# Kernel tuning notes

Measured on AMD Instinct MI355X. Metric: run time of the kernel, lower is better.

The kernel has to match this reference:

```python
import jax, jax.numpy as jnp
import numpy as np

N_NODES = 100000
N_EDGES = 1600000
IN_F = 64
HIDDEN = 128
HIDDEN2 = HIDDEN // 2
N_CLASSES = 10


def setup_inputs() -> dict:
    key = jax.random.key(0)
    ks = jax.random.split(key, 8)
    x = jax.random.normal(ks[0], (N_NODES, IN_F), dtype=jnp.float32)
    edge_index = jax.random.randint(ks[1], (2, N_EDGES), 0, N_NODES, dtype=jnp.int64 if jax.config.jax_enable_x64 else jnp.int32)
    # Linear params (PyTorch nn.Linear: y = x @ W.T + b); store as [in, out] for einsum-free matmul
    def lin(k, fi, fo):
        bound = 1.0 / np.sqrt(fi)
        kw, kb = jax.random.split(k)
        W = jax.random.uniform(kw, (fi, fo), minval=-bound, maxval=bound, dtype=jnp.float32)
        b = jax.random.uniform(kb, (fo,), minval=-bound, maxval=bound, dtype=jnp.float32)
        return W, b
    W1, b1 = lin(ks[2], IN_F, HIDDEN)
    W2, b2 = lin(ks[3], HIDDEN, HIDDEN2)
    W3, b3 = lin(ks[4], HIDDEN2, N_CLASSES)
    return {"x": x, "edge_index": edge_index, "n_nodes": N_NODES,
            "W1": W1, "b1": b1, "W2": W2, "b2": b2, "W3": W3, "b3": b3}


def gcn_layer(x, row, col, n_nodes, W, b):
    # gather source features, scatter-add into destination nodes
    agg = jax.ops.segment_sum(x[row], col, num_segments=n_nodes)  # [N, F]
    deg = jax.ops.segment_sum(jnp.ones_like(col, dtype=x.dtype), col, num_segments=n_nodes)
    deg = jnp.maximum(deg, 1.0)
    return (agg / deg[:, None]) @ W + b


def reference(x, edge_index, n_nodes, W1, b1, W2, b2, W3, b3):
    row, col = edge_index[0], edge_index[1]
    h = jax.nn.relu(gcn_layer(x, row, col, n_nodes, W1, b1))
    # dropout is identity in eval mode
    h = jax.nn.relu(gcn_layer(h, row, col, n_nodes, W2, b2))
    return h @ W3 + b3
```

## Files before the change

### kernel.cpp

```cpp
#include <hip/hip_runtime.h>

#define N_NODES 100000
#define N_EDGES 1600000
#define IN_F 64
#define HID 128
#define HID2 64
#define NCLS 10

#define SEG 64

#define NBUCK 256
#define SUBR 391
#define CAP2 7000
#define EBA 1600

typedef __attribute__((ext_vector_type(8))) short bfrag;
typedef __attribute__((ext_vector_type(4))) float f32x4;

__device__ __forceinline__ unsigned short bf_rne(float f) {
  unsigned int u = __float_as_uint(f);
  u += 0x7fffu + ((u >> 16) & 1u);
  return (unsigned short)(u >> 16);
}

__global__ __launch_bounds__(256) void cast_k(const float* __restrict__ x,
                                              unsigned short* __restrict__ xb) {
  int i = blockIdx.x * blockDim.x + threadIdx.x;
  const float4* xf4 = (const float4*)x;
  float4 a = xf4[2 * i];
  float4 b = xf4[2 * i + 1];
  ushort4 o0, o1;
  o0.x = bf_rne(a.x); o0.y = bf_rne(a.y); o0.z = bf_rne(a.z); o0.w = bf_rne(a.w);
  o1.x = bf_rne(b.x); o1.y = bf_rne(b.y); o1.z = bf_rne(b.z); o1.w = bf_rne(b.w);
  ushort4* ob = (ushort4*)xb;
  ob[2 * i] = o0;
  ob[2 * i + 1] = o1;
}

__global__ __launch_bounds__(256) void wtrans_k(const float* __restrict__ W1,
                                                const float* __restrict__ W2,
                                                unsigned short* __restrict__ W1t,
                                                unsigned short* __restrict__ W2t) {
  int i = blockIdx.x * 256 + threadIdx.x;
  if (i < IN_F * HID) {
    int j = i >> 6, k = i & 63;
    W1t[i] = bf_rne(W1[k * HID + j]);
  } else {
    int i2 = i - IN_F * HID;
    int j = i2 >> 7, k = i2 & 127;
    W2t[i2] = bf_rne(W2[k * HID2 + j]);
  }
}

__global__ __launch_bounds__(256) void binA_k(const int* __restrict__ row,
                                              const int* __restrict__ col,
                                              int* __restrict__ bcnt,
                                              unsigned int* __restrict__ pairs) {
  __shared__ int hcnt[NBUCK];
  __shared__ int hbase[NBUCK];
  int t = threadIdx.x;
  hcnt[t] = 0;
  __syncthreads();
  int e0 = blockIdx.x * EBA;
  int e1 = e0 + EBA;
  for (int e = e0 + t; e < e1; e += 256) {
    int b = col[e] / SUBR;
    atomicAdd(&hcnt[b], 1);
  }
  __syncthreads();
  hbase[t] = atomicAdd(&bcnt[t], hcnt[t]);
  hcnt[t] = 0;
  __syncthreads();
  for (int e = e0 + t; e < e1; e += 256) {
    int dst = col[e];
    int src = row[e];
    int b = dst / SUBR;
    int pos = hbase[b] + atomicAdd(&hcnt[b], 1);
    pairs[(size_t)b * CAP2 + pos] =
        ((unsigned)(dst - b * SUBR) << 17) | (unsigned)src;
  }
}

__global__ __launch_bounds__(512) void binB_k(const unsigned int* __restrict__ pairs,
                                              const int* __restrict__ bcnt,
                                              int* __restrict__ cursors,
                                              int* __restrict__ csr_src) {
  __shared__ int cur[SUBR];
  int b = blockIdx.x;
  int t = threadIdx.x;
  int lo = b * SUBR;
  for (int i = t; i < SUBR; i += 512) cur[i] = 0;
  __syncthreads();
  int cnt = bcnt[b];
  const unsigned int* bp = pairs + (size_t)b * CAP2;
  for (int i = t; i < cnt; i += 512) {
    unsigned w = bp[i];
    int local = w >> 17;
    int src = (int)(w & 0x1ffffu);
    int pos = atomicAdd(&cur[local], 1);
    if (pos < SEG) csr_src[(size_t)(lo + local) * SEG + pos] = src;
  }
  __syncthreads();
  for (int i = t; i < SUBR; i += 512) {
    int n = lo + i;
    if (n < N_NODES) {
      int d = cur[i];
      if (d > SEG) d = SEG;
      cursors[n] = n * SEG + d;
      int cons = d <= 32 ? 32 : ((d + 15) & ~15);
      for (int q = d; q < cons; q++) csr_src[(size_t)n * SEG + q] = 0;
    }
  }
}

#define ACC1(r)                                                     \
  {                                                                 \
    ax += __uint_as_float((r).x << 16);                             \
    ay += __uint_as_float((r).x & 0xffff0000u);                     \
    az += __uint_as_float((r).y << 16);                             \
    aw += __uint_as_float((r).y & 0xffff0000u);                     \
  }
#define LD8(r, ia, ib)                                              \
  {                                                                 \
    r[0] = vb[(size_t)(unsigned)(ia).x * 16 + fc];                  \
    r[1] = vb[(size_t)(unsigned)(ia).y * 16 + fc];                  \
    r[2] = vb[(size_t)(unsigned)(ia).z * 16 + fc];                  \
    r[3] = vb[(size_t)(unsigned)(ia).w * 16 + fc];                  \
    r[4] = vb[(size_t)(unsigned)(ib).x * 16 + fc];                  \
    r[5] = vb[(size_t)(unsigned)(ib).y * 16 + fc];                  \
    r[6] = vb[(size_t)(unsigned)(ib).z * 16 + fc];                  \
    r[7] = vb[(size_t)(unsigned)(ib).w * 16 + fc];                  \
  }
#define NODE_BODY(i, rbuf, dd)                                      \
  {                                                                 \
    float ax = 0.f, ay = 0.f, az = 0.f, aw = 0.f;                   \
    ACC1(rbuf[0]) ACC1(rbuf[1]) ACC1(rbuf[2]) ACC1(rbuf[3])         \
    ACC1(rbuf[4]) ACC1(rbuf[5]) ACC1(rbuf[6]) ACC1(rbuf[7])         \
    int cons = 32;                                                  \
    if (dd > 32) {                                                  \
      cons = (dd + 15) & ~15;                                       \
      int sbase = (n0 + i) * SEG;                                   \
      for (int p = sbase + 32; p < sbase + cons; p += 16) {         \
        int4 iT = csr4[(p >> 2) + eg];                              \
        uint2 t0 = vb[(size_t)(unsigned)iT.x * 16 + fc];            \
        uint2 t1 = vb[(size_t)(unsigned)iT.y * 16 + fc];            \
        uint2 t2 = vb[(size_t)(unsigned)iT.z * 16 + fc];            \
        uint2 t3 = vb[(size_t)(unsigned)iT.w * 16 + fc];            \
        ACC1(t0) ACC1(t1) ACC1(t2) ACC1(t3)                         \
      }                                                             \
    }                                                               \
    ax += __shfl_xor(ax, 16); ay += __shfl_xor(ay, 16);             \
    az += __shfl_xor(az, 16); aw += __shfl_xor(aw, 16);             \
    ax += __shfl_xor(ax, 32); ay += __shfl_xor(ay, 32);             \
    az += __shfl_xor(az, 32); aw += __shfl_xor(aw, 32);             \
    float pc = (float)(cons - dd);                                  \
    emit(i, make_float4(ax - pc * zx, ay - pc * zy,                 \
                        az - pc * zz, aw - pc * zw), dd);           \
  }

template <class F>
__device__ __forceinline__ void gather4_bf16(
    const uint2* __restrict__ vb, const int* __restrict__ csr,
    const int* __restrict__ cursors, int n0, int eg, int fc, F&& emit) {
  const int4* csr4 = (const int4*)csr;
  size_t rb = (size_t)n0 * 16;
  int4 iA0 = csr4[rb + eg];
  int4 iB0 = csr4[rb + 4 + eg];
  int4 iA1 = csr4[rb + 16 + eg];
  int4 iB1 = csr4[rb + 20 + eg];
  int4 iA2 = csr4[rb + 32 + eg];
  int4 iB2 = csr4[rb + 36 + eg];
  int4 iA3 = csr4[rb + 48 + eg];
  int4 iB3 = csr4[rb + 52 + eg];
  int d0 = cursors[n0 + 0] - (n0 + 0) * SEG;
  int d1 = cursors[n0 + 1] - (n0 + 1) * SEG;
  int d2 = cursors[n0 + 2] - (n0 + 2) * SEG;
  int d3 = cursors[n0 + 3] - (n0 + 3) * SEG;
  uint2 z = vb[fc];
  uint2 rA[8], rB[8], rC[8], rD[8];
  LD8(rA, iA0, iB0)
  LD8(rB, iA1, iB1)
  LD8(rC, iA2, iB2)
  LD8(rD, iA3, iB3)
  __builtin_amdgcn_sched_barrier(0);
  float zx = __uint_as_float(z.x << 16);
  float zy = __uint_as_float(z.x & 0xffff0000u);
  float zz = __uint_as_float(z.y << 16);
  float zw = __uint_as_float(z.y & 0xffff0000u);
  NODE_BODY(0, rA, d0)
  NODE_BODY(1, rB, d1)
  NODE_BODY(2, rC, d2)
  NODE_BODY(3, rD, d3)
}

#define NB1 32
#define XS_S 72
#define HS_S 136
__global__ __launch_bounds__(512, 4) void gmm1_k(
    const unsigned short* __restrict__ xb, const int* __restrict__ cursors,
    const int* __restrict__ csr_src, const unsigned short* __restrict__ W1t,
    const float* __restrict__ b1, const unsigned short* __restrict__ W2t,
    unsigned short* __restrict__ g) {
  __shared__ unsigned short xsb[NB1 * XS_S];
  __shared__ unsigned short hsb[NB1 * HS_S];
  int t = threadIdx.x;
  int node0 = blockIdx.x * NB1;
  int wave = t >> 6;
  int lane = t & 63;
  int eg = lane >> 4;
  int fc = lane & 15;
  {
    const uint2* vb = (const uint2*)xb;
    gather4_bf16(vb, csr_src, cursors, node0 + wave * 4, eg, fc,
                 [&](int i, float4 a, int dd) {
                   if (eg == 0) {
                     float inv = 1.0f / (dd < 1 ? 1.0f : (float)dd);
                     ushort4 o;
                     o.x = bf_rne(a.x * inv); o.y = bf_rne(a.y * inv);
                     o.z = bf_rne(a.z * inv); o.w = bf_rne(a.w * inv);
                     *(ushort4*)&xsb[(wave * 4 + i) * XS_S + fc * 4] = o;
                   }
                 });
  }
  __syncthreads();
  int lr = lane & 15;
  int kb = lane >> 4;
  {
    int col = wave * 16 + lr;
    bfrag wf0 = *(const bfrag*)&W1t[col * IN_F + kb * 8];
    bfrag wf1 = *(const bfrag*)&W1t[col * IN_F + 32 + kb * 8];
    float bb = b1[col];
#pragma unroll
    for (int m = 0; m < 2; m++) {
      f32x4 acc = {0.f, 0.f, 0.f, 0.f};
      bfrag a0 = *(const bfrag*)&xsb[(m * 16 + lr) * XS_S + kb * 8];
      bfrag a1 = *(const bfrag*)&xsb[(m * 16 + lr) * XS_S + 32 + kb * 8];
      acc = __builtin_amdgcn_mfma_f32_16x16x32_bf16(a0, wf0, acc, 0, 0, 0);
      acc = __builtin_amdgcn_mfma_f32_16x16x32_bf16(a1, wf1, acc, 0, 0, 0);
#pragma unroll
      for (int q = 0; q < 4; q++) {
        int r = m * 16 + kb * 4 + q;
        float v = acc[q] + bb;
        hsb[r * HS_S + col] = bf_rne(v > 0.0f ? v : 0.0f);
      }
    }
  }
  __syncthreads();
  {
    int m = wave >> 2;
    int col = (wave & 3) * 16 + lr;
    f32x4 acc = {0.f, 0.f, 0.f, 0.f};
#pragma unroll
    for (int s = 0; s < 4; s++) {
      bfrag af = *(const bfrag*)&hsb[(m * 16 + lr) * HS_S + s * 32 + kb * 8];
      bfrag bf = *(const bfrag*)&W2t[col * HID + s * 32 + kb * 8];
      acc = __builtin_amdgcn_mfma_f32_16x16x32_bf16(af, bf, acc, 0, 0, 0);
    }
#pragma unroll
    for (int q = 0; q < 4; q++) {
      int r = m * 16 + kb * 4 + q;
      g[(size_t)(node0 + r) * HID2 + col] = bf_rne(acc[q]);
    }
  }
}

#define NBH 32
__global__ __launch_bounds__(512, 4) void ghead_k(
    const unsigned short* __restrict__ g, const int* __restrict__ cursors,
    const int* __restrict__ csr_src, const float* __restrict__ b2,
    const float* __restrict__ W3, const float* __restrict__ b3,
    float* __restrict__ out) {
  __shared__ float W3l[HID2 * NCLS];
  __shared__ float hs[NBH][HID2 + 4];
  int t = threadIdx.x;
  for (int i = t; i < HID2 * NCLS; i += 512) W3l[i] = W3[i];
  int node0 = blockIdx.x * NBH;
  int lane = t & 63;
  int wave = t >> 6;
  int eg = lane >> 4;
  int fc = lane & 15;
  {
    const uint2* vb = (const uint2*)g;
    const float4* b2f4 = (const float4*)b2;
    float4 bb = b2f4[fc];
    gather4_bf16(vb, csr_src, cursors, node0 + wave * 4, eg, fc,
                 [&](int i, float4 a, int dd) {
                   if (eg == 0) {
                     float inv = 1.0f / (dd < 1 ? 1.0f : (float)dd);
                     float4 v;
                     v.x = a.x * inv + bb.x; v.y = a.y * inv + bb.y;
                     v.z = a.z * inv + bb.z; v.w = a.w * inv + bb.w;
                     v.x = v.x > 0.0f ? v.x : 0.0f;
                     v.y = v.y > 0.0f ? v.y : 0.0f;
                     v.z = v.z > 0.0f ? v.z : 0.0f;
                     v.w = v.w > 0.0f ? v.w : 0.0f;
                     *(float4*)&hs[wave * 4 + i][fc * 4] = v;
                   }
                 });
  }
  __syncthreads();
  if (t < NBH * NCLS) {
    int n = t / NCLS;
    int c = t - n * NCLS;
    float a = b3[c];
    for (int k = 0; k < HID2; k++) a += hs[n][k] * W3l[k * NCLS + c];
    out[(size_t)(node0 + n) * NCLS + c] = a;
  }
}

extern "C" void kernel_launch(void* const* d_in, const int* in_sizes, int n_in,
                              void* d_out, int out_size, void* d_ws, size_t ws_size,
                              hipStream_t stream) {
  const float* x  = (const float*)d_in[0];
  const int*   ei = (const int*)d_in[1];
  const int*   row = ei;
  const int*   col = ei + N_EDGES;
  const float* W1 = (const float*)d_in[3];
  const float* b1 = (const float*)d_in[4];
  const float* W2 = (const float*)d_in[5];
  const float* b2 = (const float*)d_in[6];
  const float* W3 = (const float*)d_in[7];
  const float* b3 = (const float*)d_in[8];
  float* out = (float*)d_out;

  char* ws = (char*)d_ws;
  int*            cursors = (int*)ws;
  int*            bcnt    = (int*)(ws + (512 << 10));
  unsigned short* W1t     = (unsigned short*)(ws + (520 << 10));
  unsigned short* W2t     = (unsigned short*)(ws + (552 << 10));
  int*            csr_src = (int*)(ws + (1 << 20));
  unsigned int*   pairs   = (unsigned int*)(ws + (28 << 20));
  unsigned short* xb      = (unsigned short*)(ws + (36 << 20));
  unsigned short* g       = (unsigned short*)(ws + (49 << 20));

  (void)hipMemsetAsync(bcnt, 0, NBUCK * sizeof(int), stream);
  wtrans_k<<<(IN_F * HID + HID * HID2) / 256, 256, 0, stream>>>(W1, W2, W1t, W2t);
  cast_k<<<N_NODES * IN_F / 8 / 256, 256, 0, stream>>>(x, xb);
  binA_k<<<N_EDGES / EBA, 256, 0, stream>>>(row, col, bcnt, pairs);
  binB_k<<<NBUCK, 512, 0, stream>>>(pairs, bcnt, cursors, csr_src);

  gmm1_k<<<N_NODES / NB1, 512, 0, stream>>>(xb, cursors, csr_src, W1t, b1, W2t, g);

  ghead_k<<<N_NODES / NBH, 512, 0, stream>>>(g, cursors, csr_src, b2, W3, b3, out);
}
```

Measured before the change: 157.2 us.

## Split fused gather+matmul kernels into separate gather and dense kernels

Splits the two fused gather+MFMA kernels into standalone gather kernels (256 threads, one node at a time per wave) that write mean-aggregated bf16 features to a workspace buffer, followed by separate matmul and head kernels that read them back. The aim is smaller, higher-occupancy gather kernels without the matmul's shared-memory and register footprint. It also drops the explicit batching of 32 outstanding loads per lane. In exchange it adds two kernel launches and an extra round trip of intermediate features through global memory.

Measured after the change: 166.9 us. 1.06x slower.

```diff
diff --git a/kernel.cpp b/kernel.cpp
--- a/kernel.cpp
+++ b/kernel.cpp
@@ -113,6 +113,23 @@
   }
 }
 
+__device__ __forceinline__ float4 gather_node(const uint2* __restrict__ vb,
+                                              const int4* __restrict__ csr4,
+                                              int n, int d, int eg, int fc,
+                                              float zx, float zy, float zz,
+                                              float zw) {
+  float ax = 0.f, ay = 0.f, az = 0.f, aw = 0.f;
+  int s4 = n * 16;
+  int4 ia = csr4[s4 + eg];
+  int4 ib = csr4[s4 + 4 + eg];
+  uint2 r0 = vb[(size_t)(unsigned)ia.x * 16 + fc];
+  uint2 r1 = vb[(size_t)(unsigned)ia.y * 16 + fc];
+  uint2 r2 = vb[(size_t)(unsigned)ia.z * 16 + fc];
+  uint2 r3 = vb[(size_t)(unsigned)ia.w * 16 + fc];
+  uint2 r4 = vb[(size_t)(unsigned)ib.x * 16 + fc];
+  uint2 r5 = vb[(size_t)(unsigned)ib.y * 16 + fc];
+  uint2 r6 = vb[(size_t)(unsigned)ib.z * 16 + fc];
+  uint2 r7 = vb[(size_t)(unsigned)ib.w * 16 + fc];
 #define ACC1(r)                                                     \
   {                                                                 \
     ax += __uint_as_float((r).x << 16);                             \
@@ -120,109 +137,114 @@
     az += __uint_as_float((r).y << 16);                             \
     aw += __uint_as_float((r).y & 0xffff0000u);                     \
   }
-#define LD8(r, ia, ib)                                              \
-  {                                                                 \
-    r[0] = vb[(size_t)(unsigned)(ia).x * 16 + fc];                  \
-    r[1] = vb[(size_t)(unsigned)(ia).y * 16 + fc];                  \
-    r[2] = vb[(size_t)(unsigned)(ia).z * 16 + fc];                  \
-    r[3] = vb[(size_t)(unsigned)(ia).w * 16 + fc];                  \
-    r[4] = vb[(size_t)(unsigned)(ib).x * 16 + fc];                  \
-    r[5] = vb[(size_t)(unsigned)(ib).y * 16 + fc];                  \
-    r[6] = vb[(size_t)(unsigned)(ib).z * 16 + fc];                  \
-    r[7] = vb[(size_t)(unsigned)(ib).w * 16 + fc];                  \
-  }
-#define NODE_BODY(i, rbuf, dd)                                      \
-  {                                                                 \
-    float ax = 0.f, ay = 0.f, az = 0.f, aw = 0.f;                   \
-    ACC1(rbuf[0]) ACC1(rbuf[1]) ACC1(rbuf[2]) ACC1(rbuf[3])         \
-    ACC1(rbuf[4]) ACC1(rbuf[5]) ACC1(rbuf[6]) ACC1(rbuf[7])         \
-    int cons = 32;                                                  \
-    if (dd > 32) {                                                  \
-      cons = (dd + 15) & ~15;                                       \
-      int sbase = (n0 + i) * SEG;                                   \
-      for (int p = sbase + 32; p < sbase + cons; p += 16) {         \
-        int4 iT = csr4[(p >> 2) + eg];                              \
-        uint2 t0 = vb[(size_t)(unsigned)iT.x * 16 + fc];            \
-        uint2 t1 = vb[(size_t)(unsigned)iT.y * 16 + fc];            \
-        uint2 t2 = vb[(size_t)(unsigned)iT.z * 16 + fc];            \
-        uint2 t3 = vb[(size_t)(unsigned)iT.w * 16 + fc];            \
-        ACC1(t0) ACC1(t1) ACC1(t2) ACC1(t3)                         \
-      }                                                             \
-    }                                                               \
-    ax += __shfl_xor(ax, 16); ay += __shfl_xor(ay, 16);             \
-    az += __shfl_xor(az, 16); aw += __shfl_xor(aw, 16);             \
-    ax += __shfl_xor(ax, 32); ay += __shfl_xor(ay, 32);             \
-    az += __shfl_xor(az, 32); aw += __shfl_xor(aw, 32);             \
-    float pc = (float)(cons - dd);                                  \
-    emit(i, make_float4(ax - pc * zx, ay - pc * zy,                 \
-                        az - pc * zz, aw - pc * zw), dd);           \
-  }
-
-template <class F>
-__device__ __forceinline__ void gather4_bf16(
-    const uint2* __restrict__ vb, const int* __restrict__ csr,
-    const int* __restrict__ cursors, int n0, int eg, int fc, F&& emit) {
-  const int4* csr4 = (const int4*)csr;
-  size_t rb = (size_t)n0 * 16;
-  int4 iA0 = csr4[rb + eg];
-  int4 iB0 = csr4[rb + 4 + eg];
-  int4 iA1 = csr4[rb + 16 + eg];
-  int4 iB1 = csr4[rb + 20 + eg];
-  int4 iA2 = csr4[rb + 32 + eg];
-  int4 iB2 = csr4[rb + 36 + eg];
-  int4 iA3 = csr4[rb + 48 + eg];
-  int4 iB3 = csr4[rb + 52 + eg];
-  int d0 = cursors[n0 + 0] - (n0 + 0) * SEG;
-  int d1 = cursors[n0 + 1] - (n0 + 1) * SEG;
-  int d2 = cursors[n0 + 2] - (n0 + 2) * SEG;
-  int d3 = cursors[n0 + 3] - (n0 + 3) * SEG;
+  ACC1(r0) ACC1(r1) ACC1(r2) ACC1(r3) ACC1(r4) ACC1(r5) ACC1(r6) ACC1(r7)
+  int cons = 32;
+  if (d > 32) {
+    cons = (d + 15) & ~15;
+    for (int p = n * SEG + 32; p < n * SEG + cons; p += 16) {
+      int4 it = csr4[(p >> 2) + eg];
+      uint2 t0 = vb[(size_t)(unsigned)it.x * 16 + fc];
+      uint2 t1 = vb[(size_t)(unsigned)it.y * 16 + fc];
+      uint2 t2 = vb[(size_t)(unsigned)it.z * 16 + fc];
+      uint2 t3 = vb[(size_t)(unsigned)it.w * 16 + fc];
+      ACC1(t0) ACC1(t1) ACC1(t2) ACC1(t3)
+    }
+  }
+#undef ACC1
+  ax += __shfl_xor(ax, 16); ay += __shfl_xor(ay, 16);
+  az += __shfl_xor(az, 16); aw += __shfl_xor(aw, 16);
+  ax += __shfl_xor(ax, 32); ay += __shfl_xor(ay, 32);
+  az += __shfl_xor(az, 32); aw += __shfl_xor(aw, 32);
+  float pc = (float)(cons - d);
+  return make_float4(ax - pc * zx, ay - pc * zy, az - pc * zz, aw - pc * zw);
+}
+
+__global__ __launch_bounds__(256) void gather1_k(
+    const unsigned short* __restrict__ xb, const int* __restrict__ cursors,
+    const int* __restrict__ csr_src, unsigned short* __restrict__ xm) {
+  int t = threadIdx.x;
+  int lane = t & 63;
+  int eg = lane >> 4;
+  int fc = lane & 15;
+  int n0 = (blockIdx.x * 4 + (t >> 6)) * 4;
+  const uint2* vb = (const uint2*)xb;
+  const int4* csr4 = (const int4*)csr_src;
   uint2 z = vb[fc];
-  uint2 rA[8], rB[8], rC[8], rD[8];
-  LD8(rA, iA0, iB0)
-  LD8(rB, iA1, iB1)
-  LD8(rC, iA2, iB2)
-  LD8(rD, iA3, iB3)
-  __builtin_amdgcn_sched_barrier(0);
   float zx = __uint_as_float(z.x << 16);
   float zy = __uint_as_float(z.x & 0xffff0000u);
   float zz = __uint_as_float(z.y << 16);
   float zw = __uint_as_float(z.y & 0xffff0000u);
-  NODE_BODY(0, rA, d0)
-  NODE_BODY(1, rB, d1)
-  NODE_BODY(2, rC, d2)
-  NODE_BODY(3, rD, d3)
+  for (int i = 0; i < 4; i++) {
+    int n = n0 + i;
+    int d = cursors[n] - n * SEG;
+    float4 a = gather_node(vb, csr4, n, d, eg, fc, zx, zy, zz, zw);
+    if (eg == 0) {
+      float inv = 1.0f / (d < 1 ? 1.0f : (float)d);
+      ushort4 o;
+      o.x = bf_rne(a.x * inv); o.y = bf_rne(a.y * inv);
+      o.z = bf_rne(a.z * inv); o.w = bf_rne(a.w * inv);
+      *(ushort4*)&xm[(size_t)n * IN_F + fc * 4] = o;
+    }
+  }
+}
+
+__global__ __launch_bounds__(256) void gather2_k(
+    const unsigned short* __restrict__ g, const int* __restrict__ cursors,
+    const int* __restrict__ csr_src, const float* __restrict__ b2,
+    unsigned short* __restrict__ hm) {
+  int t = threadIdx.x;
+  int lane = t & 63;
+  int eg = lane >> 4;
+  int fc = lane & 15;
+  int n0 = (blockIdx.x * 4 + (t >> 6)) * 4;
+  const uint2* vb = (const uint2*)g;
+  const int4* csr4 = (const int4*)csr_src;
+  uint2 z = vb[fc];
+  float zx = __uint_as_float(z.x << 16);
+  float zy = __uint_as_float(z.x & 0xffff0000u);
+  float zz = __uint_as_float(z.y << 16);
+  float zw = __uint_as_float(z.y & 0xffff0000u);
+  const float4* b2f4 = (const float4*)b2;
+  float4 bb = b2f4[fc];
+  for (int i = 0; i < 4; i++) {
+    int n = n0 + i;
+    int d = cursors[n] - n * SEG;
+    float4 a = gather_node(vb, csr4, n, d, eg, fc, zx, zy, zz, zw);
+    if (eg == 0) {
+      float inv = 1.0f / (d < 1 ? 1.0f : (float)d);
+      float vx = a.x * inv + bb.x;
+      float vy = a.y * inv + bb.y;
+      float vz = a.z * inv + bb.z;
+      float vw = a.w * inv + bb.w;
+      ushort4 o;
+      o.x = bf_rne(vx > 0.0f ? vx : 0.0f);
+      o.y = bf_rne(vy > 0.0f ? vy : 0.0f);
+      o.z = bf_rne(vz > 0.0f ? vz : 0.0f);
+      o.w = bf_rne(vw > 0.0f ? vw : 0.0f);
+      *(ushort4*)&hm[(size_t)n * HID2 + fc * 4] = o;
+    }
+  }
 }
 
 #define NB1 32
 #define XS_S 72
 #define HS_S 136
-__global__ __launch_bounds__(512, 4) void gmm1_k(
-    const unsigned short* __restrict__ xb, const int* __restrict__ cursors,
-    const int* __restrict__ csr_src, const unsigned short* __restrict__ W1t,
+__global__ __launch_bounds__(512) void mm12_k(
+    const unsigned short* __restrict__ xm, const unsigned short* __restrict__ W1t,
     const float* __restrict__ b1, const unsigned short* __restrict__ W2t,
     unsigned short* __restrict__ g) {
   __shared__ unsigned short xsb[NB1 * XS_S];
   __shared__ unsigned short hsb[NB1 * HS_S];
   int t = threadIdx.x;
   int node0 = blockIdx.x * NB1;
+  {
+    int r = t >> 4, u = t & 15;
+    *(ushort4*)&xsb[r * XS_S + u * 4] =
+        ((const ushort4*)xm)[(size_t)(node0 + r) * (IN_F / 4) + u];
+  }
+  __syncthreads();
   int wave = t >> 6;
   int lane = t & 63;
-  int eg = lane >> 4;
-  int fc = lane & 15;
-  {
-    const uint2* vb = (const uint2*)xb;
-    gather4_bf16(vb, csr_src, cursors, node0 + wave * 4, eg, fc,
-                 [&](int i, float4 a, int dd) {
-                   if (eg == 0) {
-                     float inv = 1.0f / (dd < 1 ? 1.0f : (float)dd);
-                     ushort4 o;
-                     o.x = bf_rne(a.x * inv); o.y = bf_rne(a.y * inv);
-                     o.z = bf_rne(a.z * inv); o.w = bf_rne(a.w * inv);
-                     *(ushort4*)&xsb[(wave * 4 + i) * XS_S + fc * 4] = o;
-                   }
-                 });
-  }
-  __syncthreads();
   int lr = lane & 15;
   int kb = lane >> 4;
   {
@@ -264,46 +286,29 @@
   }
 }
 
-#define NBH 32
-__global__ __launch_bounds__(512, 4) void ghead_k(
-    const unsigned short* __restrict__ g, const int* __restrict__ cursors,
-    const int* __restrict__ csr_src, const float* __restrict__ b2,
-    const float* __restrict__ W3, const float* __restrict__ b3,
-    float* __restrict__ out) {
+#define NBH3 25
+__global__ __launch_bounds__(256) void head_k(
+    const unsigned short* __restrict__ hm, const float* __restrict__ W3,
+    const float* __restrict__ b3, float* __restrict__ out) {
   __shared__ float W3l[HID2 * NCLS];
-  __shared__ float hs[NBH][HID2 + 4];
-  int t = threadIdx.x;
-  for (int i = t; i < HID2 * NCLS; i += 512) W3l[i] = W3[i];
-  int node0 = blockIdx.x * NBH;
-  int lane = t & 63;
-  int wave = t >> 6;
-  int eg = lane >> 4;
-  int fc = lane & 15;
-  {
-    const uint2* vb = (const uint2*)g;
-    const float4* b2f4 = (const float4*)b2;
-    float4 bb = b2f4[fc];
-    gather4_bf16(vb, csr_src, cursors, node0 + wave * 4, eg, fc,
-                 [&](int i, float4 a, int dd) {
-                   if (eg == 0) {
-                     float inv = 1.0f / (dd < 1 ? 1.0f : (float)dd);
-                     float4 v;
-                     v.x = a.x * inv + bb.x; v.y = a.y * inv + bb.y;
-                     v.z = a.z * inv + bb.z; v.w = a.w * inv + bb.w;
-                     v.x = v.x > 0.0f ? v.x : 0.0f;
-                     v.y = v.y > 0.0f ? v.y : 0.0f;
-                     v.z = v.z > 0.0f ? v.z : 0.0f;
-                     v.w = v.w > 0.0f ? v.w : 0.0f;
-                     *(float4*)&hs[wave * 4 + i][fc * 4] = v;
-                   }
-                 });
-  }
-  __syncthreads();
-  if (t < NBH * NCLS) {
+  __shared__ float hsl[NBH3][HID2 + 4];
+  int t = threadIdx.x;
+  for (int i = t; i < HID2 * NCLS; i += 256) W3l[i] = W3[i];
+  int node0 = blockIdx.x * NBH3;
+  for (int u = t; u < NBH3 * (HID2 / 4); u += 256) {
+    int r = u >> 4, c = u & 15;
+    ushort4 v = ((const ushort4*)hm)[(size_t)(node0 + r) * (HID2 / 4) + c];
+    hsl[r][c * 4 + 0] = __uint_as_float((unsigned)v.x << 16);
+    hsl[r][c * 4 + 1] = __uint_as_float((unsigned)v.y << 16);
+    hsl[r][c * 4 + 2] = __uint_as_float((unsigned)v.z << 16);
+    hsl[r][c * 4 + 3] = __uint_as_float((unsigned)v.w << 16);
+  }
+  __syncthreads();
+  if (t < NBH3 * NCLS) {
     int n = t / NCLS;
     int c = t - n * NCLS;
     float a = b3[c];
-    for (int k = 0; k < HID2; k++) a += hs[n][k] * W3l[k * NCLS + c];
+    for (int k = 0; k < HID2; k++) a += hsl[n][k] * W3l[k * NCLS + c];
     out[(size_t)(node0 + n) * NCLS + c] = a;
   }
 }
@@ -332,6 +337,8 @@
   unsigned int*   pairs   = (unsigned int*)(ws + (28 << 20));
   unsigned short* xb      = (unsigned short*)(ws + (36 << 20));
   unsigned short* g       = (unsigned short*)(ws + (49 << 20));
+  unsigned short* xm      = (unsigned short*)(ws + (62 << 20));
+  unsigned short* hm      = xm;
 
   (void)hipMemsetAsync(bcnt, 0, NBUCK * sizeof(int), stream);
   wtrans_k<<<(IN_F * HID + HID * HID2) / 256, 256, 0, stream>>>(W1, W2, W1t, W2t);
@@ -339,7 +346,9 @@
   binA_k<<<N_EDGES / EBA, 256, 0, stream>>>(row, col, bcnt, pairs);
   binB_k<<<NBUCK, 512, 0, stream>>>(pairs, bcnt, cursors, csr_src);
 
-  gmm1_k<<<N_NODES / NB1, 512, 0, stream>>>(xb, cursors, csr_src, W1t, b1, W2t, g);
-
-  ghead_k<<<N_NODES / NBH, 512, 0, stream>>>(g, cursors, csr_src, b2, W3, b3, out);
-}
+  gather1_k<<<N_NODES / 16, 256, 0, stream>>>(xb, cursors, csr_src, xm);
+  mm12_k<<<N_NODES / NB1, 512, 0, stream>>>(xm, W1t, b1, W2t, g);
+
+  gather2_k<<<N_NODES / 16, 256, 0, stream>>>(g, cursors, csr_src, b2, hm);
+  head_k<<<N_NODES / NBH3, 256, 0, stream>>>(hm, W3, b3, out);
+}
```
